# Kernel tuning notes

Measured on AMD Instinct MI355X. Metric: run time of the kernel, lower is better.

## Reference

```python
import jax, jax.numpy as jnp
import numpy as np

B, N, D = 8, 2048, 768
LN_EPS = 1e-5


def setup_inputs() -> dict:
    key = jax.random.key(0)
    ks = jax.random.split(key, 5)
    scale = 1.0 / np.sqrt(D)
    features = jax.random.normal(ks[0], (B, N, D), dtype=jnp.float32)
    mask = jax.random.randint(ks[1], (B, N), 0, 2) == 1  # True = masked (padding)
    Wq = jax.random.normal(ks[2], (D, D), dtype=jnp.float32) * scale
    Wk = jax.random.normal(ks[3], (D, D), dtype=jnp.float32) * scale
    Wv = jax.random.normal(ks[4], (D, D), dtype=jnp.float32) * scale
    ln_gamma = jnp.ones((D,), dtype=jnp.float32)
    ln_beta = jnp.zeros((D,), dtype=jnp.float32)
    return {"features": features, "mask": mask, "Wq": Wq, "Wk": Wk, "Wv": Wv,
            "ln_gamma": ln_gamma, "ln_beta": ln_beta}


def reference(features, mask, Wq, Wk, Wv, ln_gamma, ln_beta):
    # LayerNorm over last dim
    mu = jnp.mean(features, axis=-1, keepdims=True)
    var = jnp.mean(jnp.square(features - mu), axis=-1, keepdims=True)
    x = (features - mu) * jax.lax.rsqrt(var + LN_EPS) * ln_gamma + ln_beta
    # torch Linear: y = x @ W.T
    Q = jnp.einsum('bnd,ed->bne', x, Wq)
    K = jnp.einsum('bnd,ed->bne', x, Wk)
    V = jnp.einsum('bnd,ed->bne', x, Wv)
    scale = x.shape[-1] ** -0.5
    scores = jnp.einsum('bnd,bmd->bnm', Q, K) * scale  # [B,N,N]
    scores = jnp.where(mask[:, None, :], -jnp.inf, scores)
    probs = jax.nn.softmax(scores, axis=-1)
    ctx = jnp.einsum('bnm,bmd->bnd', probs, V)
    return ctx
```

## Files before the change

### kernel.cpp

```cpp
#include <hip/hip_runtime.h>
#include <hip/hip_bf16.h>
#include <cstdint>

typedef __attribute__((ext_vector_type(8))) __bf16 bf16v8;
typedef __attribute__((ext_vector_type(4))) float f32x4;
typedef __attribute__((ext_vector_type(4))) unsigned short ushort4v;
typedef __attribute__((ext_vector_type(8))) unsigned short ushort8v;

#define BB 8
#define NN 2048
#define DD 768

__device__ __forceinline__ float b2f(unsigned short u) {
  union { unsigned int i; float f; } c; c.i = ((unsigned int)u) << 16; return c.f;
}
__device__ __forceinline__ unsigned short f2b(float f) {
  union { float f; unsigned int i; } c; c.f = f;
  unsigned int u = c.i;
  return (unsigned short)((u + 0x7fffu + ((u >> 16) & 1u)) >> 16);
}

__global__ __launch_bounds__(256) void ln_kernel(const float* __restrict__ x,
                                                 const float* __restrict__ gamma,
                                                 const float* __restrict__ beta,
                                                 unsigned short* __restrict__ xb) {
  int row = blockIdx.x;
  const float* xr = x + (size_t)row * DD;
  int t = threadIdx.x;
  float a0 = xr[t], a1 = xr[t + 256], a2 = xr[t + 512];
  float s = a0 + a1 + a2;
  float q = a0 * a0 + a1 * a1 + a2 * a2;
  for (int o = 32; o > 0; o >>= 1) { s += __shfl_xor(s, o); q += __shfl_xor(q, o); }
  __shared__ float red[2][4];
  int w = t >> 6, lane = t & 63;
  if (lane == 0) { red[0][w] = s; red[1][w] = q; }
  __syncthreads();
  s = red[0][0] + red[0][1] + red[0][2] + red[0][3];
  q = red[1][0] + red[1][1] + red[1][2] + red[1][3];
  float mean = s * (1.0f / DD);
  float var = q * (1.0f / DD) - mean * mean;
  float inv = rsqrtf(var + 1e-5f);
  unsigned short* o0 = xb + (size_t)row * DD;
  o0[t]       = f2b((a0 - mean) * inv * gamma[t]       + beta[t]);
  o0[t + 256] = f2b((a1 - mean) * inv * gamma[t + 256] + beta[t + 256]);
  o0[t + 512] = f2b((a2 - mean) * inv * gamma[t + 512] + beta[t + 512]);
}

__global__ __launch_bounds__(256) void wconvert(const float* __restrict__ Wq,
                                                const float* __restrict__ Wk,
                                                const float* __restrict__ Wv,
                                                unsigned short* __restrict__ Wcat) {
  int i = blockIdx.x * 256 + threadIdx.x;
  const int dd = DD * DD;
  if (i >= 3 * dd) return;
  float v;
  if (i < dd)           v = Wq[i] * 0.03608439182435161f;
  else if (i < 2 * dd)  v = Wk[i - dd];
  else                  v = Wv[i - 2 * dd];
  Wcat[i] = f2b(v);
}

__device__ __forceinline__ void gload_lds16(const void* g, void* l) {
  __builtin_amdgcn_global_load_lds(
      (const __attribute__((address_space(1))) void*)g,
      (__attribute__((address_space(3))) void*)(unsigned)(uintptr_t)l,
      16, 0, 0);
}

#define RDA(i0, ks, B)                                                                   \
  _Pragma("unroll")                                                                      \
  for (int i_ = 0; i_ < 4; ++i_)                                                         \
    aq[i_] = *(const bf16v8*)&smem[(B) + (ks) * 8192 + arow0 + ((i0) + i_) * 512 + kg8];
#define RDB(ks, B)                                                                       \
  _Pragma("unroll")                                                                      \
  for (int j_ = 0; j_ < NJ; ++j_)                                                        \
    bq[j_] = *(const bf16v8*)&smem[(B) + 16384 + (ks) * 8192 + brow0 + j_ * 512 + kg8];
#define MFQ(i0)                                                                          \
  _Pragma("unroll")                                                                      \
  for (int i_ = 0; i_ < 4; ++i_) {                                                       \
    _Pragma("unroll")                                                                    \
    for (int j_ = 0; j_ < NJ; ++j_)                                                      \
      acc[(i0) + i_][j_] = __builtin_amdgcn_mfma_f32_16x16x32_bf16(                      \
          aq[i_], bq[j_], acc[(i0) + i_][j_], 0, 0, 0);                                  \
  }
#define BARF asm volatile("s_barrier" ::: "memory")
#define VMC6 asm volatile("s_waitcnt vmcnt(6)" ::: "memory")
#define VMC0 asm volatile("s_waitcnt vmcnt(0)" ::: "memory")
#define P1   __builtin_amdgcn_s_setprio(1)
#define P0   __builtin_amdgcn_s_setprio(0)

#define TILEK(KT, CURB, NXTB)                                                            \
  do {                                                                                   \
                                                   \
    RDA(0, 0, CURB); RDB(0, CURB);                                                       \
    if ((KT) + 1 < NT) stgA((KT) + 1, 1, (NXTB));                                        \
    BARF; P1; MFQ(0); P0; BARF;                                                          \
                                       \
    RDA(4, 0, CURB);                                                                     \
    if ((KT) + 1 < NT) stgB((KT) + 1, 1, (NXTB));                                        \
    BARF; P1; MFQ(4); P0;                                                                \
    VMC6; BARF;                                                                          \
                                                   \
    RDA(0, 1, CURB); RDB(1, CURB);                                                       \
    if ((KT) + 2 < NT) stgA((KT) + 2, 0, (CURB));                                        \
    BARF; P1; MFQ(0); P0; BARF;                                                          \
                                                   \
    RDA(4, 1, CURB);                                                                     \
    if ((KT) + 2 < NT) stgB((KT) + 2, 0, (CURB));                                        \
    BARF; P1; MFQ(4); P0;                                                                \
    if ((KT) < NT - 2) { VMC6; } else { VMC0; }                                          \
    BARF;                                                                                \
  } while (0)

template <int MODE, int NJ>
__global__ __launch_bounds__(512, 2) void gemm256(
    const unsigned short* __restrict__ A, const unsigned short* __restrict__ Bm,
    unsigned short* __restrict__ Cq, unsigned short* __restrict__ Ck,
    unsigned short* __restrict__ Cv, float* __restrict__ Cf,
    int K, int lda, int ldb,
    long aStride, long bStride, long cStride) {
  extern __shared__ unsigned short smem[];
  const int BN = NJ * 64;

  const int t = threadIdx.x;
  int bx = blockIdx.x, by = blockIdx.y, bz = blockIdx.z;
  {
    const int gx = gridDim.x, gy = gridDim.y;
    const int nwg = gx * gy * (int)gridDim.z;
    int id = bx + gx * (by + gy * bz);
    int sw = (id & 7) * (nwg >> 3) + (id >> 3);
    bx = sw % gx; int r2 = sw / gx;
    by = r2 % gy; bz = r2 / gy;
  }
  const int n0 = bx * BN, m0 = by * 256;
  const unsigned short* Ab = A + (size_t)bz * aStride;
  const unsigned short* Bb = Bm + (size_t)bz * bStride;

  const int lane = t & 63;
  const int w = t >> 6;
  const int wm = w >> 2, wn = w & 3;
  const int frow = lane & 15;
  const int kg8 = (lane >> 4) * 8;
  const int arow0 = (wm * 128 + frow) * 32;
  const int brow0 = (wn * (NJ * 16) + frow) * 32;

  const unsigned short* Asrc = Ab + (size_t)(m0 + (t >> 2)) * lda + (t & 3) * 8;
  const unsigned short* Bsrc = Bb + (size_t)(n0 + (t >> 2)) * ldb + (t & 3) * 8;
  const int sdst = w * 512;

  auto stgA = [&](int kt, int ks, int bufb) {
    const unsigned short* s = Asrc + kt * 64 + ks * 32;
    gload_lds16(s, &smem[bufb + ks * 8192 + sdst]);
    gload_lds16(s + (size_t)128 * lda, &smem[bufb + ks * 8192 + 4096 + sdst]);
  };
  auto stgB = [&](int kt, int ks, int bufb) {
    const unsigned short* s = Bsrc + kt * 64 + ks * 32;
    gload_lds16(s, &smem[bufb + 16384 + ks * 8192 + sdst]);
    gload_lds16(s + (size_t)128 * ldb, &smem[bufb + 16384 + ks * 8192 + 4096 + sdst]);
  };

  f32x4 acc[8][NJ] = {};
  const int NT = K >> 6;
  bf16v8 aq[4], bq[NJ];

  stgA(0, 0, 0);     stgB(0, 0, 0);
  stgA(0, 1, 0);     stgB(0, 1, 0);
  stgA(1, 0, 32768); stgB(1, 0, 32768);
  asm volatile("s_waitcnt vmcnt(8)" ::: "memory");
  BARF;

  for (int ktp = 0; ktp < NT; ktp += 2) {
    TILEK(ktp, 0, 32768);
    TILEK(ktp + 1, 32768, 0);
  }

  const int r0 = (lane >> 4) * 4;
  const int c0 = lane & 15;
  const int mrowB = m0 + wm * 128 + r0;
  const int ncolB = n0 + wn * (NJ * 16) + c0;

  if (MODE == 0) {
    if (n0 < 1536) {
      unsigned short* dst = (n0 < 768) ? Cq : Ck;
      const int cb = (n0 < 768) ? 0 : 768;
#pragma unroll
      for (int i = 0; i < 8; ++i)
#pragma unroll
        for (int j = 0; j < NJ; ++j)
#pragma unroll
          for (int r = 0; r < 4; ++r)
            dst[(size_t)(mrowB + i * 16 + r) * DD + (ncolB + j * 16 - cb)] = f2b(acc[i][j][r]);
    } else {
#pragma unroll
      for (int i = 0; i < 8; ++i) {
        int row = mrowB + i * 16;
        int bb = row >> 11, nn = row & 2047;
#pragma unroll
        for (int j = 0; j < NJ; ++j) {
          int e = ncolB + j * 16 - 1536;
          ushort4v pk;
#pragma unroll
          for (int r = 0; r < 4; ++r) pk[r] = f2b(acc[i][j][r]);
          *(ushort4v*)&Cv[((size_t)(bb * DD + e)) * NN + nn] = pk;
        }
      }
    }
  } else if (MODE == 1) {
    unsigned short* dst = Cq + (size_t)bz * cStride;
#pragma unroll
    for (int i = 0; i < 8; ++i)
#pragma unroll
      for (int j = 0; j < NJ; ++j)
#pragma unroll
        for (int r = 0; r < 4; ++r)
          dst[(size_t)(mrowB + i * 16 + r) * NN + (ncolB + j * 16)] = f2b(acc[i][j][r]);
  } else {
    float* dst = Cf + (size_t)bz * cStride;
#pragma unroll
    for (int i = 0; i < 8; ++i)
#pragma unroll
      for (int j = 0; j < NJ; ++j)
#pragma unroll
        for (int r = 0; r < 4; ++r)
          dst[(size_t)(mrowB + i * 16 + r) * DD + (ncolB + j * 16)] = acc[i][j][r];
  }
}

__global__ __launch_bounds__(256) void softmax_mask(unsigned short* __restrict__ S,
                                                    const int* __restrict__ mask) {
  int row = blockIdx.x;
  int bb = row >> 11;
  unsigned short* sr = S + (size_t)row * NN;
  const int* mr = mask + bb * NN;
  int t = threadIdx.x;

  ushort8v pk = *(const ushort8v*)&sr[t * 8];
  float v[8];
  int msk[8];
#pragma unroll
  for (int j = 0; j < 8; ++j) msk[j] = mr[t * 8 + j];
  float mx = -1e30f;
#pragma unroll
  for (int j = 0; j < 8; ++j) {
    v[j] = b2f(pk[j]);
    if (!msk[j]) mx = fmaxf(mx, v[j]);
  }
  for (int o = 32; o > 0; o >>= 1) mx = fmaxf(mx, __shfl_xor(mx, o));
  __shared__ float redm[4], reds[4];
  int w = t >> 6, lane = t & 63;
  if (lane == 0) redm[w] = mx;
  __syncthreads();
  mx = fmaxf(fmaxf(redm[0], redm[1]), fmaxf(redm[2], redm[3]));

  float e[8];
  float sum = 0.f;
#pragma unroll
  for (int j = 0; j < 8; ++j) {
    e[j] = msk[j] ? 0.f : __expf(v[j] - mx);
    sum += e[j];
  }
  for (int o = 32; o > 0; o >>= 1) sum += __shfl_xor(sum, o);
  if (lane == 0) reds[w] = sum;
  __syncthreads();
  sum = reds[0] + reds[1] + reds[2] + reds[3];
  float inv = 1.0f / sum;

  ushort8v op;
#pragma unroll
  for (int j = 0; j < 8; ++j) op[j] = f2b(e[j] * inv);
  *(ushort8v*)&sr[t * 8] = op;
}

extern "C" void kernel_launch(void* const* d_in, const int* in_sizes, int n_in,
                              void* d_out, int out_size, void* d_ws, size_t ws_size,
                              hipStream_t stream) {
  const float* features = (const float*)d_in[0];
  const int* mask       = (const int*)d_in[1];
  const float* Wq       = (const float*)d_in[2];
  const float* Wk       = (const float*)d_in[3];
  const float* Wv       = (const float*)d_in[4];
  const float* gamma    = (const float*)d_in[5];
  const float* beta     = (const float*)d_in[6];
  float* out = (float*)d_out;

  char* ws = (char*)d_ws;
  size_t off = 0;
  auto alloc = [&](size_t bytes) {
    char* p = ws + off;
    off += (bytes + 255) & ~(size_t)255;
    return p;
  };
  unsigned short* Wcat = (unsigned short*)alloc((size_t)(2304 + 64) * DD * 2);
  unsigned short* Qb   = (unsigned short*)alloc((size_t)BB * NN * DD * 2);
  unsigned short* Kb   = (unsigned short*)alloc((size_t)BB * NN * DD * 2);
  unsigned short* Vt   = (unsigned short*)alloc(((size_t)BB * DD + 64) * NN * 2);
  char* last = alloc((size_t)BB * NN * NN * 2);
  unsigned short* Sb = (unsigned short*)last;
  unsigned short* Xb = (unsigned short*)last;

  (void)hipFuncSetAttribute(reinterpret_cast<const void*>(&gemm256<0, 3>),
                            hipFuncAttributeMaxDynamicSharedMemorySize, 131072);
  (void)hipFuncSetAttribute(reinterpret_cast<const void*>(&gemm256<1, 4>),
                            hipFuncAttributeMaxDynamicSharedMemorySize, 131072);
  (void)hipFuncSetAttribute(reinterpret_cast<const void*>(&gemm256<2, 3>),
                            hipFuncAttributeMaxDynamicSharedMemorySize, 131072);

  ln_kernel<<<BB * NN, 256, 0, stream>>>(features, gamma, beta, Xb);
  wconvert<<<(3 * DD * DD + 255) / 256, 256, 0, stream>>>(Wq, Wk, Wv, Wcat);

  gemm256<0, 3><<<dim3(2304 / 192, (BB * NN) / 256, 1), 512, 131072, stream>>>(
      Xb, Wcat, Qb, Kb, Vt, nullptr, DD, DD, DD, 0, 0, 0);

  gemm256<1, 4><<<dim3(NN / 256, NN / 256, BB), 512, 131072, stream>>>(
      Qb, Kb, Sb, nullptr, nullptr, nullptr, DD, DD, DD,
      (long)NN * DD, (long)NN * DD, (long)NN * NN);

  softmax_mask<<<BB * NN, 256, 0, stream>>>(Sb, mask);

  gemm256<2, 3><<<dim3(DD / 192, NN / 256, BB), 512, 131072, stream>>>(
      Sb, Vt, nullptr, nullptr, nullptr, out, NN, NN, NN,
      (long)NN * NN, (long)DD * NN, (long)NN * DD);
}
```

Before: 241.5 us.

## Make GEMMs persistent-style with 256 workgroups looping over multiple N tiles

Replaces the multi-dimensional grids of the three GEMMs with a fixed 256-workgroup launch, where each workgroup loops over several N tiles and keeps the A tile rows fixed. The K pipeline now runs continuously across tile boundaries, so the next tile's loads overlap the current tile's tail, with an epilogue write and accumulator reset between tiles. The aim is to fill the GPU in a single wave, avoid tail waves, and cut launch/prologue overhead. In exchange the epilogue stores are serialized inside the loop, and the index mapping is hardcoded for these shapes.

```diff
diff --git a/kernel.cpp b/kernel.cpp
--- a/kernel.cpp
+++ b/kernel.cpp
@@ -93,46 +93,42 @@
   do {                                                                                   \
                                                    \
     RDA(0, 0, CURB); RDB(0, CURB);                                                       \
-    if ((KT) + 1 < NT) stgA((KT) + 1, 1, (NXTB));                                        \
+    if ((KT) + 1 < NTtot) stgA((KT) + 1, 1, (NXTB));                                     \
     BARF; P1; MFQ(0); P0; BARF;                                                          \
                                        \
     RDA(4, 0, CURB);                                                                     \
-    if ((KT) + 1 < NT) stgB((KT) + 1, 1, (NXTB));                                        \
+    if ((KT) + 1 < NTtot) stgB((KT) + 1, 1, (NXTB));                                     \
     BARF; P1; MFQ(4); P0;                                                                \
     VMC6; BARF;                                                                          \
                                                    \
     RDA(0, 1, CURB); RDB(1, CURB);                                                       \
-    if ((KT) + 2 < NT) stgA((KT) + 2, 0, (CURB));                                        \
+    if ((KT) + 2 < NTtot) stgA((KT) + 2, 0, (CURB));                                     \
     BARF; P1; MFQ(0); P0; BARF;                                                          \
                                                    \
     RDA(4, 1, CURB);                                                                     \
-    if ((KT) + 2 < NT) stgB((KT) + 2, 0, (CURB));                                        \
+    if ((KT) + 2 < NTtot) stgB((KT) + 2, 0, (CURB));                                     \
     BARF; P1; MFQ(4); P0;                                                                \
-    if ((KT) < NT - 2) { VMC6; } else { VMC0; }                                          \
+    if ((KT) < NTtot - 2) { VMC6; } else { VMC0; }                                       \
     BARF;                                                                                \
   } while (0)
 
-template <int MODE, int NJ>
-__global__ __launch_bounds__(512, 2) void gemm256(
+template <int MODE, int NJ, int NTT, int TPB, int NSTEP, int IDXB>
+__global__ __launch_bounds__(512, 2) void gemmP(
     const unsigned short* __restrict__ A, const unsigned short* __restrict__ Bm,
     unsigned short* __restrict__ Cq, unsigned short* __restrict__ Ck,
     unsigned short* __restrict__ Cv, float* __restrict__ Cf,
-    int K, int lda, int ldb,
+    int lda, int ldb,
     long aStride, long bStride, long cStride) {
   extern __shared__ unsigned short smem[];
-  const int BN = NJ * 64;
+  constexpr int BN = NJ * 64;
+  constexpr int NTtot = NTT * TPB;
 
   const int t = threadIdx.x;
-  int bx = blockIdx.x, by = blockIdx.y, bz = blockIdx.z;
-  {
-    const int gx = gridDim.x, gy = gridDim.y;
-    const int nwg = gx * gy * (int)gridDim.z;
-    int id = bx + gx * (by + gy * bz);
-    int sw = (id & 7) * (nwg >> 3) + (id >> 3);
-    bx = sw % gx; int r2 = sw / gx;
-    by = r2 % gy; bz = r2 / gy;
-  }
-  const int n0 = bx * BN, m0 = by * 256;
+  const int lid = (blockIdx.x & 7) * 32 + (blockIdx.x >> 3);
+  const int bz = lid / IDXB;
+  const int idx = lid % IDXB;
+  const int m0 = (idx >> 2) * 256;
+  const int n0b = (idx & 3) * BN;
   const unsigned short* Ab = A + (size_t)bz * aStride;
   const unsigned short* Bb = Bm + (size_t)bz * bStride;
 
@@ -144,24 +140,81 @@
   const int arow0 = (wm * 128 + frow) * 32;
   const int brow0 = (wn * (NJ * 16) + frow) * 32;
 
-  const unsigned short* Asrc = Ab + (size_t)(m0 + (t >> 2)) * lda + (t & 3) * 8;
-  const unsigned short* Bsrc = Bb + (size_t)(n0 + (t >> 2)) * ldb + (t & 3) * 8;
+  const int srow = t >> 2;
+  const int scol8 = (t & 3) * 8;
+  const unsigned short* AsrcB = Ab + (size_t)(m0 + srow) * lda + scol8;
+  const unsigned short* BsrcB = Bb + (size_t)(n0b + srow) * ldb + scol8;
+  const size_t bTileStep = (size_t)NSTEP * ldb;
   const int sdst = w * 512;
 
-  auto stgA = [&](int kt, int ks, int bufb) {
-    const unsigned short* s = Asrc + kt * 64 + ks * 32;
+  auto stgA = [&](int kq, int ks, int bufb) {
+    const int kk = kq % NTT;
+    const unsigned short* s = AsrcB + kk * 64 + ks * 32;
     gload_lds16(s, &smem[bufb + ks * 8192 + sdst]);
     gload_lds16(s + (size_t)128 * lda, &smem[bufb + ks * 8192 + 4096 + sdst]);
   };
-  auto stgB = [&](int kt, int ks, int bufb) {
-    const unsigned short* s = Bsrc + kt * 64 + ks * 32;
+  auto stgB = [&](int kq, int ks, int bufb) {
+    const int tt = kq / NTT, kk = kq % NTT;
+    const unsigned short* s = BsrcB + (size_t)tt * bTileStep + kk * 64 + ks * 32;
     gload_lds16(s, &smem[bufb + 16384 + ks * 8192 + sdst]);
     gload_lds16(s + (size_t)128 * ldb, &smem[bufb + 16384 + ks * 8192 + 4096 + sdst]);
   };
 
   f32x4 acc[8][NJ] = {};
-  const int NT = K >> 6;
   bf16v8 aq[4], bq[NJ];
+
+  const int r0 = (lane >> 4) * 4;
+  const int c0 = lane & 15;
+  const int mrowB = m0 + wm * 128 + r0;
+  auto writeC = [&](int tt) {
+    const int n0w = n0b + tt * NSTEP;
+    const int ncolB = n0w + wn * (NJ * 16) + c0;
+    if (MODE == 0) {
+      if (n0w < 1536) {
+        unsigned short* dst = (n0w < 768) ? Cq : Ck;
+        const int cb = (n0w < 768) ? 0 : 768;
+#pragma unroll
+        for (int i = 0; i < 8; ++i)
+#pragma unroll
+          for (int j = 0; j < NJ; ++j)
+#pragma unroll
+            for (int r = 0; r < 4; ++r)
+              dst[(size_t)(mrowB + i * 16 + r) * DD + (ncolB + j * 16 - cb)] = f2b(acc[i][j][r]);
+      } else {
+#pragma unroll
+        for (int i = 0; i < 8; ++i) {
+          int row = mrowB + i * 16;
+          int bb = row >> 11, nn = row & 2047;
+#pragma unroll
+          for (int j = 0; j < NJ; ++j) {
+            int e = ncolB + j * 16 - 1536;
+            ushort4v pk;
+#pragma unroll
+            for (int r = 0; r < 4; ++r) pk[r] = f2b(acc[i][j][r]);
+            *(ushort4v*)&Cv[((size_t)(bb * DD + e)) * NN + nn] = pk;
+          }
+        }
+      }
+    } else if (MODE == 1) {
+      unsigned short* dst = Cq + (size_t)bz * cStride;
+#pragma unroll
+      for (int i = 0; i < 8; ++i)
+#pragma unroll
+        for (int j = 0; j < NJ; ++j)
+#pragma unroll
+          for (int r = 0; r < 4; ++r)
+            dst[(size_t)(mrowB + i * 16 + r) * NN + (ncolB + j * 16)] = f2b(acc[i][j][r]);
+    } else {
+      float* dst = Cf + (size_t)bz * cStride;
+#pragma unroll
+      for (int i = 0; i < 8; ++i)
+#pragma unroll
+        for (int j = 0; j < NJ; ++j)
+#pragma unroll
+          for (int r = 0; r < 4; ++r)
+            dst[(size_t)(mrowB + i * 16 + r) * DD + (ncolB + j * 16)] = acc[i][j][r];
+    }
+  };
 
   stgA(0, 0, 0);     stgB(0, 0, 0);
   stgA(0, 1, 0);     stgB(0, 1, 0);
@@ -169,60 +222,16 @@
   asm volatile("s_waitcnt vmcnt(8)" ::: "memory");
   BARF;
 
-  for (int ktp = 0; ktp < NT; ktp += 2) {
-    TILEK(ktp, 0, 32768);
-    TILEK(ktp + 1, 32768, 0);
-  }
-
-  const int r0 = (lane >> 4) * 4;
-  const int c0 = lane & 15;
-  const int mrowB = m0 + wm * 128 + r0;
-  const int ncolB = n0 + wn * (NJ * 16) + c0;
-
-  if (MODE == 0) {
-    if (n0 < 1536) {
-      unsigned short* dst = (n0 < 768) ? Cq : Ck;
-      const int cb = (n0 < 768) ? 0 : 768;
+  for (int q = 0; q < NTtot; q += 2) {
+    TILEK(q, 0, 32768);
+    TILEK(q + 1, 32768, 0);
+    if (((q + 2) % NTT) == 0) {
+      writeC((q + 2) / NTT - 1);
 #pragma unroll
       for (int i = 0; i < 8; ++i)
 #pragma unroll
-        for (int j = 0; j < NJ; ++j)
-#pragma unroll
-          for (int r = 0; r < 4; ++r)
-            dst[(size_t)(mrowB + i * 16 + r) * DD + (ncolB + j * 16 - cb)] = f2b(acc[i][j][r]);
-    } else {
-#pragma unroll
-      for (int i = 0; i < 8; ++i) {
-        int row = mrowB + i * 16;
-        int bb = row >> 11, nn = row & 2047;
-#pragma unroll
-        for (int j = 0; j < NJ; ++j) {
-          int e = ncolB + j * 16 - 1536;
-          ushort4v pk;
-#pragma unroll
-          for (int r = 0; r < 4; ++r) pk[r] = f2b(acc[i][j][r]);
-          *(ushort4v*)&Cv[((size_t)(bb * DD + e)) * NN + nn] = pk;
-        }
-      }
+        for (int j = 0; j < NJ; ++j) acc[i][j] = f32x4{0.f, 0.f, 0.f, 0.f};
     }
-  } else if (MODE == 1) {
-    unsigned short* dst = Cq + (size_t)bz * cStride;
-#pragma unroll
-    for (int i = 0; i < 8; ++i)
-#pragma unroll
-      for (int j = 0; j < NJ; ++j)
-#pragma unroll
-        for (int r = 0; r < 4; ++r)
-          dst[(size_t)(mrowB + i * 16 + r) * NN + (ncolB + j * 16)] = f2b(acc[i][j][r]);
-  } else {
-    float* dst = Cf + (size_t)bz * cStride;
-#pragma unroll
-    for (int i = 0; i < 8; ++i)
-#pragma unroll
-      for (int j = 0; j < NJ; ++j)
-#pragma unroll
-        for (int r = 0; r < 4; ++r)
-          dst[(size_t)(mrowB + i * 16 + r) * DD + (ncolB + j * 16)] = acc[i][j][r];
   }
 }
 
@@ -298,26 +307,26 @@
   unsigned short* Sb = (unsigned short*)last;
   unsigned short* Xb = (unsigned short*)last;
 
-  (void)hipFuncSetAttribute(reinterpret_cast<const void*>(&gemm256<0, 3>),
+  (void)hipFuncSetAttribute(reinterpret_cast<const void*>(&gemmP<0, 3, 12, 3, 768, 256>),
                             hipFuncAttributeMaxDynamicSharedMemorySize, 131072);
-  (void)hipFuncSetAttribute(reinterpret_cast<const void*>(&gemm256<1, 4>),
+  (void)hipFuncSetAttribute(reinterpret_cast<const void*>(&gemmP<1, 4, 12, 2, 1024, 32>),
                             hipFuncAttributeMaxDynamicSharedMemorySize, 131072);
-  (void)hipFuncSetAttribute(reinterpret_cast<const void*>(&gemm256<2, 3>),
+  (void)hipFuncSetAttribute(reinterpret_cast<const void*>(&gemmP<2, 3, 32, 1, 0, 32>),
                             hipFuncAttributeMaxDynamicSharedMemorySize, 131072);
 
   ln_kernel<<<BB * NN, 256, 0, stream>>>(features, gamma, beta, Xb);
   wconvert<<<(3 * DD * DD + 255) / 256, 256, 0, stream>>>(Wq, Wk, Wv, Wcat);
 
-  gemm256<0, 3><<<dim3(2304 / 192, (BB * NN) / 256, 1), 512, 131072, stream>>>(
-      Xb, Wcat, Qb, Kb, Vt, nullptr, DD, DD, DD, 0, 0, 0);
-
-  gemm256<1, 4><<<dim3(NN / 256, NN / 256, BB), 512, 131072, stream>>>(
-      Qb, Kb, Sb, nullptr, nullptr, nullptr, DD, DD, DD,
+  gemmP<0, 3, 12, 3, 768, 256><<<256, 512, 131072, stream>>>(
+      Xb, Wcat, Qb, Kb, Vt, nullptr, DD, DD, 0, 0, 0);
+
+  gemmP<1, 4, 12, 2, 1024, 32><<<256, 512, 131072, stream>>>(
+      Qb, Kb, Sb, nullptr, nullptr, nullptr, DD, DD,
       (long)NN * DD, (long)NN * DD, (long)NN * NN);
 
   softmax_mask<<<BB * NN, 256, 0, stream>>>(Sb, mask);
 
-  gemm256<2, 3><<<dim3(DD / 192, NN / 256, BB), 512, 131072, stream>>>(
-      Sb, Vt, nullptr, nullptr, nullptr, out, NN, NN, NN,
+  gemmP<2, 3, 32, 1, 0, 32><<<256, 512, 131072, stream>>>(
+      Sb, Vt, nullptr, nullptr, nullptr, out, NN, NN,
       (long)NN * NN, (long)DD * NN, (long)NN * DD);
 }
```

Result: slower. 275.4 us (+14.0%).

## Make GEMMs persistent with 256 workgroups, compile-time K trip count, LDS-staged V transpose

Applied to the files above, without the earlier changes.

Replaces the per-tile grid launch with a fixed 256-workgroup persistent grid in which each workgroup loops over several output tiles, using a static XCD-aware mapping. The K-loop trip count becomes a template constant so it can be unrolled. The transposed V output is now staged through LDS and written as 16-byte coalesced rows instead of scattered 8-byte stores. The aim is to cut wave-quantization tail effects, launch/scheduling overhead and uncoalesced stores, at the cost of extra barriers and a rigid tile-to-workgroup mapping tied to the fixed shapes.

```diff
diff --git a/kernel.cpp b/kernel.cpp
--- a/kernel.cpp
+++ b/kernel.cpp
@@ -91,20 +91,16 @@
 
 #define TILEK(KT, CURB, NXTB)                                                            \
   do {                                                                                   \
-                                                   \
     RDA(0, 0, CURB); RDB(0, CURB);                                                       \
     if ((KT) + 1 < NT) stgA((KT) + 1, 1, (NXTB));                                        \
     BARF; P1; MFQ(0); P0; BARF;                                                          \
-                                       \
     RDA(4, 0, CURB);                                                                     \
     if ((KT) + 1 < NT) stgB((KT) + 1, 1, (NXTB));                                        \
     BARF; P1; MFQ(4); P0;                                                                \
     VMC6; BARF;                                                                          \
-                                                   \
     RDA(0, 1, CURB); RDB(1, CURB);                                                       \
     if ((KT) + 2 < NT) stgA((KT) + 2, 0, (CURB));                                        \
     BARF; P1; MFQ(0); P0; BARF;                                                          \
-                                                   \
     RDA(4, 1, CURB);                                                                     \
     if ((KT) + 2 < NT) stgB((KT) + 2, 0, (CURB));                                        \
     BARF; P1; MFQ(4); P0;                                                                \
@@ -112,29 +108,18 @@
     BARF;                                                                                \
   } while (0)
 
-template <int MODE, int NJ>
-__global__ __launch_bounds__(512, 2) void gemm256(
+template <int MODE, int NJ, int NTT, int TPB>
+__global__ __launch_bounds__(512, 2) void gemmT(
     const unsigned short* __restrict__ A, const unsigned short* __restrict__ Bm,
     unsigned short* __restrict__ Cq, unsigned short* __restrict__ Ck,
     unsigned short* __restrict__ Cv, float* __restrict__ Cf,
-    int K, int lda, int ldb,
+    int lda, int ldb,
     long aStride, long bStride, long cStride) {
   extern __shared__ unsigned short smem[];
-  const int BN = NJ * 64;
+  constexpr int NT = NTT;
 
   const int t = threadIdx.x;
-  int bx = blockIdx.x, by = blockIdx.y, bz = blockIdx.z;
-  {
-    const int gx = gridDim.x, gy = gridDim.y;
-    const int nwg = gx * gy * (int)gridDim.z;
-    int id = bx + gx * (by + gy * bz);
-    int sw = (id & 7) * (nwg >> 3) + (id >> 3);
-    bx = sw % gx; int r2 = sw / gx;
-    by = r2 % gy; bz = r2 / gy;
-  }
-  const int n0 = bx * BN, m0 = by * 256;
-  const unsigned short* Ab = A + (size_t)bz * aStride;
-  const unsigned short* Bb = Bm + (size_t)bz * bStride;
+  const int lid = (blockIdx.x & 7) * 32 + (blockIdx.x >> 3);
 
   const int lane = t & 63;
   const int w = t >> 6;
@@ -143,86 +128,112 @@
   const int kg8 = (lane >> 4) * 8;
   const int arow0 = (wm * 128 + frow) * 32;
   const int brow0 = (wn * (NJ * 16) + frow) * 32;
-
-  const unsigned short* Asrc = Ab + (size_t)(m0 + (t >> 2)) * lda + (t & 3) * 8;
-  const unsigned short* Bsrc = Bb + (size_t)(n0 + (t >> 2)) * ldb + (t & 3) * 8;
+  const int srow = t >> 2;
+  const int scol8 = (t & 3) * 8;
   const int sdst = w * 512;
-
-  auto stgA = [&](int kt, int ks, int bufb) {
-    const unsigned short* s = Asrc + kt * 64 + ks * 32;
-    gload_lds16(s, &smem[bufb + ks * 8192 + sdst]);
-    gload_lds16(s + (size_t)128 * lda, &smem[bufb + ks * 8192 + 4096 + sdst]);
-  };
-  auto stgB = [&](int kt, int ks, int bufb) {
-    const unsigned short* s = Bsrc + kt * 64 + ks * 32;
-    gload_lds16(s, &smem[bufb + 16384 + ks * 8192 + sdst]);
-    gload_lds16(s + (size_t)128 * ldb, &smem[bufb + 16384 + ks * 8192 + 4096 + sdst]);
-  };
-
-  f32x4 acc[8][NJ] = {};
-  const int NT = K >> 6;
-  bf16v8 aq[4], bq[NJ];
-
-  stgA(0, 0, 0);     stgB(0, 0, 0);
-  stgA(0, 1, 0);     stgB(0, 1, 0);
-  stgA(1, 0, 32768); stgB(1, 0, 32768);
-  asm volatile("s_waitcnt vmcnt(8)" ::: "memory");
-  BARF;
-
-  for (int ktp = 0; ktp < NT; ktp += 2) {
-    TILEK(ktp, 0, 32768);
-    TILEK(ktp + 1, 32768, 0);
-  }
-
   const int r0 = (lane >> 4) * 4;
   const int c0 = lane & 15;
-  const int mrowB = m0 + wm * 128 + r0;
-  const int ncolB = n0 + wn * (NJ * 16) + c0;
-
-  if (MODE == 0) {
-    if (n0 < 1536) {
-      unsigned short* dst = (n0 < 768) ? Cq : Ck;
-      const int cb = (n0 < 768) ? 0 : 768;
+
+  f32x4 acc[8][NJ];
+  bf16v8 aq[4], bq[NJ];
+
+#pragma unroll 1
+  for (int tt = 0; tt < TPB; ++tt) {
+    const int T = lid * TPB + tt;
+    int m0, n0, bz;
+    if (MODE == 0)      { bz = 0;      n0 = (T >> 6) * 192;        m0 = (T & 63) * 256; }
+    else if (MODE == 1) { bz = T >> 6; m0 = ((T >> 3) & 7) * 256;  n0 = (T & 7) * 256; }
+    else                { bz = T >> 5; m0 = ((T >> 2) & 7) * 256;  n0 = (T & 3) * 192; }
+
+    const unsigned short* AsrcB = A + (size_t)bz * aStride + (size_t)(m0 + srow) * lda + scol8;
+    const unsigned short* BsrcB = Bm + (size_t)bz * bStride + (size_t)(n0 + srow) * ldb + scol8;
+
+    auto stgA = [&](int kt, int ks, int bufb) {
+      const unsigned short* s = AsrcB + kt * 64 + ks * 32;
+      gload_lds16(s, &smem[bufb + ks * 8192 + sdst]);
+      gload_lds16(s + (size_t)128 * lda, &smem[bufb + ks * 8192 + 4096 + sdst]);
+    };
+    auto stgB = [&](int kt, int ks, int bufb) {
+      const unsigned short* s = BsrcB + kt * 64 + ks * 32;
+      gload_lds16(s, &smem[bufb + 16384 + ks * 8192 + sdst]);
+      gload_lds16(s + (size_t)128 * ldb, &smem[bufb + 16384 + ks * 8192 + 4096 + sdst]);
+    };
+
+#pragma unroll
+    for (int i = 0; i < 8; ++i)
+#pragma unroll
+      for (int j = 0; j < NJ; ++j) acc[i][j] = f32x4{0.f, 0.f, 0.f, 0.f};
+
+    stgA(0, 0, 0);     stgB(0, 0, 0);
+    stgA(0, 1, 0);     stgB(0, 1, 0);
+    stgA(1, 0, 32768); stgB(1, 0, 32768);
+    asm volatile("s_waitcnt vmcnt(8)" ::: "memory");
+    BARF;
+
+    for (int ktp = 0; ktp < NT; ktp += 2) {
+      TILEK(ktp, 0, 32768);
+      TILEK(ktp + 1, 32768, 0);
+    }
+
+    const int mrowB = m0 + wm * 128 + r0;
+    const int ncolB = n0 + wn * (NJ * 16) + c0;
+
+    if (MODE == 0) {
+      if (n0 < 1536) {
+        unsigned short* dst = (n0 < 768) ? Cq : Ck;
+        const int cb = (n0 < 768) ? 0 : 768;
+#pragma unroll
+        for (int i = 0; i < 8; ++i)
+#pragma unroll
+          for (int j = 0; j < NJ; ++j)
+#pragma unroll
+            for (int r = 0; r < 4; ++r)
+              dst[(size_t)(mrowB + i * 16 + r) * DD + (ncolB + j * 16 - cb)] = f2b(acc[i][j][r]);
+      } else {
+        BARF;
+#pragma unroll
+        for (int i = 0; i < 8; ++i)
+#pragma unroll
+          for (int j = 0; j < NJ; ++j) {
+            const int nl = wn * (NJ * 16) + j * 16 + c0;
+            const int ml = wm * 128 + i * 16 + r0;
+            ushort4v pk;
+#pragma unroll
+            for (int r = 0; r < 4; ++r) pk[r] = f2b(acc[i][j][r]);
+            *(ushort4v*)&smem[nl * 264 + ml] = pk;
+          }
+        BARF;
+        const int bb = m0 >> 11, nnb = m0 & 2047;
+        const int e0 = n0 - 1536;
+#pragma unroll
+        for (int ii = 0; ii < 12; ++ii) {
+          const int flat = t + ii * 512;
+          const int e = flat >> 5;
+          const int mo = (flat & 31) * 8;
+          ushort8v vv = *(const ushort8v*)&smem[e * 264 + mo];
+          *(ushort8v*)&Cv[((size_t)(bb * DD + e0 + e)) * NN + nnb + mo] = vv;
+        }
+        BARF;
+      }
+    } else if (MODE == 1) {
+      unsigned short* dst = Cq + (size_t)bz * cStride;
 #pragma unroll
       for (int i = 0; i < 8; ++i)
 #pragma unroll
         for (int j = 0; j < NJ; ++j)
 #pragma unroll
           for (int r = 0; r < 4; ++r)
-            dst[(size_t)(mrowB + i * 16 + r) * DD + (ncolB + j * 16 - cb)] = f2b(acc[i][j][r]);
+            dst[(size_t)(mrowB + i * 16 + r) * NN + (ncolB + j * 16)] = f2b(acc[i][j][r]);
     } else {
-#pragma unroll
-      for (int i = 0; i < 8; ++i) {
-        int row = mrowB + i * 16;
-        int bb = row >> 11, nn = row & 2047;
-#pragma unroll
-        for (int j = 0; j < NJ; ++j) {
-          int e = ncolB + j * 16 - 1536;
-          ushort4v pk;
-#pragma unroll
-          for (int r = 0; r < 4; ++r) pk[r] = f2b(acc[i][j][r]);
-          *(ushort4v*)&Cv[((size_t)(bb * DD + e)) * NN + nn] = pk;
-        }
-      }
+      float* dst = Cf + (size_t)bz * cStride;
+#pragma unroll
+      for (int i = 0; i < 8; ++i)
+#pragma unroll
+        for (int j = 0; j < NJ; ++j)
+#pragma unroll
+          for (int r = 0; r < 4; ++r)
+            dst[(size_t)(mrowB + i * 16 + r) * DD + (ncolB + j * 16)] = acc[i][j][r];
     }
-  } else if (MODE == 1) {
-    unsigned short* dst = Cq + (size_t)bz * cStride;
-#pragma unroll
-    for (int i = 0; i < 8; ++i)
-#pragma unroll
-      for (int j = 0; j < NJ; ++j)
-#pragma unroll
-        for (int r = 0; r < 4; ++r)
-          dst[(size_t)(mrowB + i * 16 + r) * NN + (ncolB + j * 16)] = f2b(acc[i][j][r]);
-  } else {
-    float* dst = Cf + (size_t)bz * cStride;
-#pragma unroll
-    for (int i = 0; i < 8; ++i)
-#pragma unroll
-      for (int j = 0; j < NJ; ++j)
-#pragma unroll
-        for (int r = 0; r < 4; ++r)
-          dst[(size_t)(mrowB + i * 16 + r) * DD + (ncolB + j * 16)] = acc[i][j][r];
   }
 }
 
@@ -298,26 +309,26 @@
   unsigned short* Sb = (unsigned short*)last;
   unsigned short* Xb = (unsigned short*)last;
 
-  (void)hipFuncSetAttribute(reinterpret_cast<const void*>(&gemm256<0, 3>),
+  (void)hipFuncSetAttribute(reinterpret_cast<const void*>(&gemmT<0, 3, 12, 3>),
                             hipFuncAttributeMaxDynamicSharedMemorySize, 131072);
-  (void)hipFuncSetAttribute(reinterpret_cast<const void*>(&gemm256<1, 4>),
+  (void)hipFuncSetAttribute(reinterpret_cast<const void*>(&gemmT<1, 4, 12, 2>),
                             hipFuncAttributeMaxDynamicSharedMemorySize, 131072);
-  (void)hipFuncSetAttribute(reinterpret_cast<const void*>(&gemm256<2, 3>),
+  (void)hipFuncSetAttribute(reinterpret_cast<const void*>(&gemmT<2, 3, 32, 1>),
                             hipFuncAttributeMaxDynamicSharedMemorySize, 131072);
 
   ln_kernel<<<BB * NN, 256, 0, stream>>>(features, gamma, beta, Xb);
   wconvert<<<(3 * DD * DD + 255) / 256, 256, 0, stream>>>(Wq, Wk, Wv, Wcat);
 
-  gemm256<0, 3><<<dim3(2304 / 192, (BB * NN) / 256, 1), 512, 131072, stream>>>(
-      Xb, Wcat, Qb, Kb, Vt, nullptr, DD, DD, DD, 0, 0, 0);
-
-  gemm256<1, 4><<<dim3(NN / 256, NN / 256, BB), 512, 131072, stream>>>(
-      Qb, Kb, Sb, nullptr, nullptr, nullptr, DD, DD, DD,
+  gemmT<0, 3, 12, 3><<<256, 512, 131072, stream>>>(
+      Xb, Wcat, Qb, Kb, Vt, nullptr, DD, DD, 0, 0, 0);
+
+  gemmT<1, 4, 12, 2><<<256, 512, 131072, stream>>>(
+      Qb, Kb, Sb, nullptr, nullptr, nullptr, DD, DD,
       (long)NN * DD, (long)NN * DD, (long)NN * NN);
 
   softmax_mask<<<BB * NN, 256, 0, stream>>>(Sb, mask);
 
-  gemm256<2, 3><<<dim3(DD / 192, NN / 256, BB), 512, 131072, stream>>>(
-      Sb, Vt, nullptr, nullptr, nullptr, out, NN, NN, NN,
+  gemmT<2, 3, 32, 1><<<256, 512, 131072, stream>>>(
+      Sb, Vt, nullptr, nullptr, nullptr, out, NN, NN,
       (long)NN * NN, (long)DD * NN, (long)NN * DD);
 }
```

Result: slower. 277.4 us (+14.9%).

## Make QKV projection GEMM persistent over multiple N-tiles with cross-tile prefetch

Applied to the files above, without the earlier changes.

Replaces the QKV projection GEMM launch (768 workgroups) with a 256-workgroup kernel where each workgroup keeps its A row-block and walks three consecutive 192-wide N segments. The next segment's B tiles are prefetched during the last K-steps of the current one, so the pipeline does not drain and refill between tiles, and the grid fits in one wave of 2 workgroups per CU. The intent is to remove tail and prologue overhead and improve A reuse in L2. The cost is a serialized epilogue store between segments, which stalls the MFMA pipeline while the writes go out.

```diff
diff --git a/kernel.cpp b/kernel.cpp
--- a/kernel.cpp
+++ b/kernel.cpp
@@ -91,24 +91,39 @@
 
 #define TILEK(KT, CURB, NXTB)                                                            \
   do {                                                                                   \
-                                                   \
     RDA(0, 0, CURB); RDB(0, CURB);                                                       \
     if ((KT) + 1 < NT) stgA((KT) + 1, 1, (NXTB));                                        \
     BARF; P1; MFQ(0); P0; BARF;                                                          \
-                                       \
     RDA(4, 0, CURB);                                                                     \
     if ((KT) + 1 < NT) stgB((KT) + 1, 1, (NXTB));                                        \
     BARF; P1; MFQ(4); P0;                                                                \
     VMC6; BARF;                                                                          \
-                                                   \
     RDA(0, 1, CURB); RDB(1, CURB);                                                       \
     if ((KT) + 2 < NT) stgA((KT) + 2, 0, (CURB));                                        \
     BARF; P1; MFQ(0); P0; BARF;                                                          \
-                                                   \
     RDA(4, 1, CURB);                                                                     \
     if ((KT) + 2 < NT) stgB((KT) + 2, 0, (CURB));                                        \
     BARF; P1; MFQ(4); P0;                                                                \
     if ((KT) < NT - 2) { VMC6; } else { VMC0; }                                          \
+    BARF;                                                                                \
+  } while (0)
+
+#define TILEKS(CURB, NXTB, S1OK, S1KK, S2OK, S2KK, BB1, BB2, TAILV)                      \
+  do {                                                                                   \
+    RDA(0, 0, CURB); RDB(0, CURB);                                                       \
+    if (S1OK) stgA((S1KK), 1, (NXTB));                                                   \
+    BARF; P1; MFQ(0); P0; BARF;                                                          \
+    RDA(4, 0, CURB);                                                                     \
+    if (S1OK) stgB((BB1), (S1KK), 1, (NXTB));                                            \
+    BARF; P1; MFQ(4); P0;                                                                \
+    VMC6; BARF;                                                                          \
+    RDA(0, 1, CURB); RDB(1, CURB);                                                       \
+    if (S2OK) stgA((S2KK), 0, (CURB));                                                   \
+    BARF; P1; MFQ(0); P0; BARF;                                                          \
+    RDA(4, 1, CURB);                                                                     \
+    if (S2OK) stgB((BB2), (S2KK), 0, (CURB));                                            \
+    BARF; P1; MFQ(4); P0;                                                                \
+    TAILV;                                                                               \
     BARF;                                                                                \
   } while (0)
 
@@ -144,8 +159,10 @@
   const int arow0 = (wm * 128 + frow) * 32;
   const int brow0 = (wn * (NJ * 16) + frow) * 32;
 
-  const unsigned short* Asrc = Ab + (size_t)(m0 + (t >> 2)) * lda + (t & 3) * 8;
-  const unsigned short* Bsrc = Bb + (size_t)(n0 + (t >> 2)) * ldb + (t & 3) * 8;
+  const int srow = t >> 2;
+  const int scol8 = (t & 3) * 8;
+  const unsigned short* Asrc = Ab + (size_t)(m0 + srow) * lda + scol8;
+  const unsigned short* Bsrc = Bb + (size_t)(n0 + srow) * ldb + scol8;
   const int sdst = w * 512;
 
   auto stgA = [&](int kt, int ks, int bufb) {
@@ -179,33 +196,7 @@
   const int mrowB = m0 + wm * 128 + r0;
   const int ncolB = n0 + wn * (NJ * 16) + c0;
 
-  if (MODE == 0) {
-    if (n0 < 1536) {
-      unsigned short* dst = (n0 < 768) ? Cq : Ck;
-      const int cb = (n0 < 768) ? 0 : 768;
-#pragma unroll
-      for (int i = 0; i < 8; ++i)
-#pragma unroll
-        for (int j = 0; j < NJ; ++j)
-#pragma unroll
-          for (int r = 0; r < 4; ++r)
-            dst[(size_t)(mrowB + i * 16 + r) * DD + (ncolB + j * 16 - cb)] = f2b(acc[i][j][r]);
-    } else {
-#pragma unroll
-      for (int i = 0; i < 8; ++i) {
-        int row = mrowB + i * 16;
-        int bb = row >> 11, nn = row & 2047;
-#pragma unroll
-        for (int j = 0; j < NJ; ++j) {
-          int e = ncolB + j * 16 - 1536;
-          ushort4v pk;
-#pragma unroll
-          for (int r = 0; r < 4; ++r) pk[r] = f2b(acc[i][j][r]);
-          *(ushort4v*)&Cv[((size_t)(bb * DD + e)) * NN + nn] = pk;
-        }
-      }
-    }
-  } else if (MODE == 1) {
+  if (MODE == 1) {
     unsigned short* dst = Cq + (size_t)bz * cStride;
 #pragma unroll
     for (int i = 0; i < 8; ++i)
@@ -223,6 +214,114 @@
 #pragma unroll
         for (int r = 0; r < 4; ++r)
           dst[(size_t)(mrowB + i * 16 + r) * DD + (ncolB + j * 16)] = acc[i][j][r];
+  }
+}
+
+template <int MODE, int NJ, int NTT, int SEGS>
+__global__ __launch_bounds__(512, 2) void gemmS(
+    const unsigned short* __restrict__ A, const unsigned short* __restrict__ Bm,
+    unsigned short* __restrict__ Cq, unsigned short* __restrict__ Ck,
+    unsigned short* __restrict__ Cv, float* __restrict__ Cf,
+    int lda, int ldb) {
+  extern __shared__ unsigned short smem[];
+  constexpr int NSTEP = NJ * 64;
+
+  const int t = threadIdx.x;
+  const int lid = (blockIdx.x & 7) * 32 + (blockIdx.x >> 3);
+  const int m0 = (lid & 63) * 256;
+  const int n0base = (lid >> 6) * (SEGS * NSTEP);
+
+  const int lane = t & 63;
+  const int w = t >> 6;
+  const int wm = w >> 2, wn = w & 3;
+  const int frow = lane & 15;
+  const int kg8 = (lane >> 4) * 8;
+  const int arow0 = (wm * 128 + frow) * 32;
+  const int brow0 = (wn * (NJ * 16) + frow) * 32;
+  const int srow = t >> 2;
+  const int scol8 = (t & 3) * 8;
+  const int sdst = w * 512;
+
+  const unsigned short* AsrcB = A + (size_t)(m0 + srow) * lda + scol8;
+  const unsigned short* Bsrc0 = Bm + (size_t)(n0base + srow) * ldb + scol8;
+
+  auto stgA = [&](int kk, int ks, int bufb) {
+    const unsigned short* s = AsrcB + kk * 64 + ks * 32;
+    gload_lds16(s, &smem[bufb + ks * 8192 + sdst]);
+    gload_lds16(s + (size_t)128 * lda, &smem[bufb + ks * 8192 + 4096 + sdst]);
+  };
+  auto stgB = [&](const unsigned short* bb_, int kk, int ks, int bufb) {
+    const unsigned short* s = bb_ + kk * 64 + ks * 32;
+    gload_lds16(s, &smem[bufb + 16384 + ks * 8192 + sdst]);
+    gload_lds16(s + (size_t)128 * ldb, &smem[bufb + 16384 + ks * 8192 + 4096 + sdst]);
+  };
+
+  f32x4 acc[8][NJ] = {};
+  bf16v8 aq[4], bq[NJ];
+  const int r0 = (lane >> 4) * 4;
+  const int c0 = lane & 15;
+  const int mrowB = m0 + wm * 128 + r0;
+
+  stgA(0, 0, 0);     stgB(Bsrc0, 0, 0, 0);
+  stgA(0, 1, 0);     stgB(Bsrc0, 0, 1, 0);
+  stgA(1, 0, 32768); stgB(Bsrc0, 1, 0, 32768);
+  asm volatile("s_waitcnt vmcnt(8)" ::: "memory");
+  BARF;
+
+#pragma unroll
+  for (int s = 0; s < SEGS; ++s) {
+    const unsigned short* Bcur = Bsrc0 + (size_t)s * NSTEP * ldb;
+    const unsigned short* Bnxt = Bcur + (size_t)NSTEP * ldb;
+    const bool hn = (s + 1 < SEGS);
+    const bool lastSeg = !hn;
+
+    for (int ktp = 0; ktp < NTT - 2; ktp += 2) {
+      TILEKS(0,     32768, true, ktp + 1, true, ktp + 2, Bcur, Bcur, VMC6);
+      TILEKS(32768, 0,     true, ktp + 2, true, ktp + 3, Bcur, Bcur, VMC6);
+    }
+    if (lastSeg) {
+      TILEKS(0,     32768, true, NTT - 1, false, 0, Bcur, Bnxt, VMC0);
+      TILEKS(32768, 0,     false, 0,      false, 1, Bnxt, Bnxt, VMC0);
+    } else {
+      TILEKS(0,     32768, true, NTT - 1, true, 0, Bcur, Bnxt, VMC6);
+      TILEKS(32768, 0,     true, 0,       true, 1, Bnxt, Bnxt, VMC6);
+    }
+
+    {
+      const int n0 = n0base + s * NSTEP;
+      const int ncolB = n0 + wn * (NJ * 16) + c0;
+      if (n0 < 1536) {
+        unsigned short* dst = (n0 < 768) ? Cq : Ck;
+        const int cb = (n0 < 768) ? 0 : 768;
+#pragma unroll
+        for (int i = 0; i < 8; ++i)
+#pragma unroll
+          for (int j = 0; j < NJ; ++j)
+#pragma unroll
+            for (int r = 0; r < 4; ++r)
+              dst[(size_t)(mrowB + i * 16 + r) * DD + (ncolB + j * 16 - cb)] = f2b(acc[i][j][r]);
+      } else {
+#pragma unroll
+        for (int i = 0; i < 8; ++i) {
+          int row = mrowB + i * 16;
+          int bb = row >> 11, nn = row & 2047;
+#pragma unroll
+          for (int j = 0; j < NJ; ++j) {
+            int e = ncolB + j * 16 - 1536;
+            ushort4v pk;
+#pragma unroll
+            for (int r = 0; r < 4; ++r) pk[r] = f2b(acc[i][j][r]);
+            *(ushort4v*)&Cv[((size_t)(bb * DD + e)) * NN + nn] = pk;
+          }
+        }
+      }
+      if (hn) {
+#pragma unroll
+        for (int i = 0; i < 8; ++i)
+#pragma unroll
+          for (int j = 0; j < NJ; ++j) acc[i][j] = f32x4{0.f, 0.f, 0.f, 0.f};
+      }
+    }
   }
 }
 
@@ -298,7 +397,7 @@
   unsigned short* Sb = (unsigned short*)last;
   unsigned short* Xb = (unsigned short*)last;
 
-  (void)hipFuncSetAttribute(reinterpret_cast<const void*>(&gemm256<0, 3>),
+  (void)hipFuncSetAttribute(reinterpret_cast<const void*>(&gemmS<0, 3, 12, 3>),
                             hipFuncAttributeMaxDynamicSharedMemorySize, 131072);
   (void)hipFuncSetAttribute(reinterpret_cast<const void*>(&gemm256<1, 4>),
                             hipFuncAttributeMaxDynamicSharedMemorySize, 131072);
@@ -308,8 +407,8 @@
   ln_kernel<<<BB * NN, 256, 0, stream>>>(features, gamma, beta, Xb);
   wconvert<<<(3 * DD * DD + 255) / 256, 256, 0, stream>>>(Wq, Wk, Wv, Wcat);
 
-  gemm256<0, 3><<<dim3(2304 / 192, (BB * NN) / 256, 1), 512, 131072, stream>>>(
-      Xb, Wcat, Qb, Kb, Vt, nullptr, DD, DD, DD, 0, 0, 0);
+  gemmS<0, 3, 12, 3><<<256, 512, 131072, stream>>>(
+      Xb, Wcat, Qb, Kb, Vt, nullptr, DD, DD);
 
   gemm256<1, 4><<<dim3(NN / 256, NN / 256, BB), 512, 131072, stream>>>(
       Qb, Kb, Sb, nullptr, nullptr, nullptr, DD, DD, DD,
```

Result: slower. 252.7 us (+4.6%).
